# Kernel optimization log

Hardware: AMD Instinct MI355X
Metric: run time of the kernel (lower is better)

The kernel has to match this reference:

```python
import math
import jax, jax.numpy as jnp
import numpy as np

B, T, C, H, V = 2, 512, 768, 12, 50304
HD = C // H
EPS_LN = 1e-5
SINK_ITERS = 6           # MAX_ITER_SINK
N_STEPS = 20             # ceil((1-0)/h_max), h_max=0.05
H_STEP = 1.0 / N_STEPS   # Euler step size h


def layer_norm(x, w, b):
    mu = jnp.mean(x, axis=-1, keepdims=True)
    var = jnp.mean(jnp.square(x - mu), axis=-1, keepdims=True)
    return (x - mu) * jax.lax.rsqrt(var + EPS_LN) * w + b


def sinkhorn_pi(Cmat):
    # log-domain Sinkhorn (eps=1) on cost matrix Cmat [N, T, T]; returns transport plan pi
    n = Cmat.shape[-1]
    log_marg = -jnp.log(jnp.asarray(n, Cmat.dtype))  # log(1/n), uniform marginals
    u = jnp.zeros(Cmat.shape[:-1], Cmat.dtype)
    v = jnp.zeros(Cmat.shape[:-1], Cmat.dtype)
    def M(u, v):
        return -Cmat + u[..., :, None] + v[..., None, :]
    for _ in range(SINK_ITERS):
        u = (log_marg - jax.nn.logsumexp(M(u, v), axis=-1)) + u
        v = (log_marg - jax.nn.logsumexp(M(u, v), axis=-2)) + v
    return jnp.exp(M(u, v))


def block_f(z, t, attn_ln_w, attn_ln_b, c_attn_w, c_attn_b, c_proj_w, c_proj_b,
            mlp_ln_w, mlp_ln_b, c_fc_w, c_fc_b, mlp_proj_w, mlp_proj_b):
    Bz, Tz, Cz = z.shape
    tcol = jnp.full((Bz, Tz, 1), t, z.dtype)
    # attention sub-block: LN over C+1 dims (x concat time)
    x = layer_norm(jnp.concatenate([z, tcol], axis=-1), attn_ln_w, attn_ln_b)
    qkv = x @ c_attn_w + c_attn_b                      # [B,T,3C]
    q, k, v = jnp.split(qkv, 3, axis=-1)
    q = q.reshape(Bz, Tz, H, HD).transpose(0, 2, 1, 3)  # [B,H,T,hd]
    k = k.reshape(Bz, Tz, H, HD).transpose(0, 2, 1, 3)
    v = v.reshape(Bz, Tz, H, HD).transpose(0, 2, 1, 3)
    att = jnp.einsum('bhqd,bhkd->bhqk', q, k) * (1.0 / math.sqrt(HD))
    mask = jnp.tril(jnp.ones((Tz, Tz), dtype=bool))
    att = jax.nn.softmax(jnp.where(mask, att, -jnp.inf), axis=-1)
    pi = sinkhorn_pi(att.reshape(Bz * H, Tz, Tz)) * Tz  # sink(att)[0] * n
    y = jnp.einsum('bhqk,bhkd->bhqd', pi.reshape(Bz, H, Tz, Tz), v)
    y = y.transpose(0, 2, 1, 3).reshape(Bz, Tz, Cz)
    y = y @ c_proj_w + c_proj_b
    # MLP sub-block on LN(concat(attn_out, t))
    ht = layer_norm(jnp.concatenate([y, tcol], axis=-1), mlp_ln_w, mlp_ln_b)
    h1 = jax.nn.gelu(ht @ c_fc_w + c_fc_b, approximate=False)
    return h1 @ mlp_proj_w + mlp_proj_b


def setup_inputs() -> dict:
    key = jax.random.key(0)
    ks = jax.random.split(key, 8)
    s = 0.02
    return {
        'idx': jax.random.randint(ks[0], (B, T), 0, V),
        'wte': s * jax.random.normal(ks[1], (V, C), jnp.float32),
        'wpe': s * jax.random.normal(ks[2], (T, C), jnp.float32),
        'attn_ln_w': jnp.ones((C + 1,), jnp.float32),
        'attn_ln_b': jnp.zeros((C + 1,), jnp.float32),
        'c_attn_w': s * jax.random.normal(ks[3], (C + 1, 3 * C), jnp.float32),
        'c_attn_b': jnp.zeros((3 * C,), jnp.float32),
        'c_proj_w': s * jax.random.normal(ks[4], (C, C), jnp.float32),
        'c_proj_b': jnp.zeros((C,), jnp.float32),
        'mlp_ln_w': jnp.ones((C + 1,), jnp.float32),
        'mlp_ln_b': jnp.zeros((C + 1,), jnp.float32),
        'c_fc_w': s * jax.random.normal(ks[5], (C + 1, 4 * C), jnp.float32),
        'c_fc_b': jnp.zeros((4 * C,), jnp.float32),
        'mlp_proj_w': s * jax.random.normal(ks[6], (4 * C, C), jnp.float32),
        'mlp_proj_b': jnp.zeros((C,), jnp.float32),
        'lnf_w': jnp.ones((C,), jnp.float32),
        'lnf_b': jnp.zeros((C,), jnp.float32),
    }


def reference(idx, wte, wpe, attn_ln_w, attn_ln_b, c_attn_w, c_attn_b, c_proj_w,
              c_proj_b, mlp_ln_w, mlp_ln_b, c_fc_w, c_fc_b, mlp_proj_w, mlp_proj_b,
              lnf_w, lnf_b):
    x = wte[idx] + wpe[jnp.arange(idx.shape[1])]  # [B,T,C]

    def step(carry, _):
        z, t = carry
        dz = block_f(z, t, attn_ln_w, attn_ln_b, c_attn_w, c_attn_b, c_proj_w,
                     c_proj_b, mlp_ln_w, mlp_ln_b, c_fc_w, c_fc_b, mlp_proj_w,
                     mlp_proj_b)
        return (z + H_STEP * dz, t + H_STEP), None

    (x, _), _ = jax.lax.scan(step, (x, jnp.float32(0.0)), None, length=N_STEPS)
    x = layer_norm(x, lnf_w, lnf_b)
    logits = x[:, -1:, :] @ wte.T  # inference path: last position only, tied head
    return logits
```

## Files before the change

### kernel.cpp

```cpp
#include <hip/hip_runtime.h>
#include <hip/hip_bf16.h>
#include <math.h>

typedef unsigned short ushortT;
typedef unsigned int uintT;

#define Bc   2
#define Tc   512
#define Cc   768
#define Hc   12
#define HDc  64
#define Vc   50304
#define BTc  (Bc*Tc)
#define NHc  (Bc*Hc)
#define C3   (3*Cc)
#define C4   (4*Cc)
#define EPS_LN 1e-5f
#define H_STEP 0.05f
#define INVN (1.0f/512.0f)
#define SB   4
#define ELP  (Tc + 8)

typedef float f32x4 __attribute__((ext_vector_type(4)));
typedef __bf16 bf16x8 __attribute__((ext_vector_type(8)));
typedef ushortT us8 __attribute__((ext_vector_type(8)));
typedef uintT u32x4 __attribute__((ext_vector_type(4)));

__device__ __forceinline__ ushortT f2bf(float f) {
    union { float f; unsigned u; } x; x.f = f;
    unsigned r = (x.u + 0x7fffu + ((x.u >> 16) & 1u)) >> 16;
    return (ushortT)r;
}
__device__ __forceinline__ float bf2f(ushortT b) {
    union { unsigned u; float f; } x; x.u = ((unsigned)b) << 16;
    return x.f;
}
__device__ __forceinline__ float bflo(uintT w) {
    union { unsigned u; float f; } x; x.u = w << 16;
    return x.f;
}
__device__ __forceinline__ float bfhi(uintT w) {
    union { unsigned u; float f; } x; x.u = w & 0xffff0000u;
    return x.f;
}

__device__ __forceinline__ void gll16(const ushortT* g, ushortT* l) {
    __builtin_amdgcn_global_load_lds(
        (const __attribute__((address_space(1))) unsigned int*)g,
        (__attribute__((address_space(3))) unsigned int*)l,
        16, 0, 0);
}

__device__ __forceinline__ float waveReduceSumX(float v) {
    for (int o = 32; o; o >>= 1) v += __shfl_xor(v, o);
    return v;
}
__device__ __forceinline__ float blockReduceSum(float v) {
    __shared__ float sm[4];
    for (int o = 32; o; o >>= 1) v += __shfl_down(v, o);
    __syncthreads();
    if ((threadIdx.x & 63) == 0) sm[threadIdx.x >> 6] = v;
    __syncthreads();
    return sm[0] + sm[1] + sm[2] + sm[3];
}

__global__ __launch_bounds__(256)
void wtrans_kernel(const float* __restrict__ W, ushortT* __restrict__ out,
                   int K, int N)
{
    __shared__ float t[32][33];
    int k0 = blockIdx.x * 32, n0 = blockIdx.y * 32;
    int tx = threadIdx.x & 31, ty = threadIdx.x >> 5;
    for (int r = ty; r < 32; r += 8)
        t[r][tx] = W[(size_t)(k0 + r) * N + n0 + tx];
    __syncthreads();
    for (int r = ty; r < 32; r += 8)
        out[(size_t)(n0 + r) * K + k0 + tx] = f2bf(t[tx][r]);
}

__global__ __launch_bounds__(256)
void embed_ln(const int* __restrict__ idx, const float* __restrict__ wte,
              const float* __restrict__ wpe, float* __restrict__ z,
              const float* __restrict__ lnw, const float* __restrict__ lnb,
              ushortT* __restrict__ xlnb, float* __restrict__ xt)
{
    int row = blockIdx.x, tid = threadIdx.x;
    int tok = idx[row];
    float v[3];
#pragma unroll
    for (int q = 0; q < 3; ++q) {
        int c = tid + 256 * q;
        float val = wte[(size_t)tok * Cc + c] + wpe[(size_t)(row & (Tc - 1)) * Cc + c];
        z[(size_t)row * Cc + c] = val;
        v[q] = val;
    }
    float s = blockReduceSum(v[0] + v[1] + v[2]);
    float mu = s / 769.f;
    float d0 = v[0] - mu, d1 = v[1] - mu, d2 = v[2] - mu;
    float ss = blockReduceSum(d0 * d0 + d1 * d1 + d2 * d2);
    float dt = 0.f - mu;
    float var = (ss + dt * dt) / 769.f;
    float rs = rsqrtf(var + EPS_LN);
#pragma unroll
    for (int q = 0; q < 3; ++q) {
        int c = tid + 256 * q;
        xlnb[(size_t)row * Cc + c] = f2bf((v[q] - mu) * rs * lnw[c] + lnb[c]);
    }
    if (tid == 0) xt[row] = dt * rs * lnw[Cc] + lnb[Cc];
}

__global__ __launch_bounds__(256)
void ln_kernel(const void* __restrict__ X, const float* __restrict__ w,
               const float* __restrict__ bb, void* __restrict__ Y,
               float* __restrict__ yt, int hasT, float tval,
               int rowMul, int rowAdd, int obf16, int ibf16)
{
    int orow = blockIdx.x;
    int r = orow * rowMul + rowAdd;
    int tid = threadIdx.x;
    float xv[3];
    if (ibf16) {
        const ushortT* x = (const ushortT*)X + (size_t)r * Cc;
#pragma unroll
        for (int q = 0; q < 3; ++q) xv[q] = bf2f(x[tid + 256 * q]);
    } else {
        const float* x = (const float*)X + (size_t)r * Cc;
#pragma unroll
        for (int q = 0; q < 3; ++q) xv[q] = x[tid + 256 * q];
    }
    float s = blockReduceSum(xv[0] + xv[1] + xv[2]);
    float cnt = hasT ? 769.f : 768.f;
    float mu = (s + (hasT ? tval : 0.f)) / cnt;
    float d0 = xv[0] - mu, d1 = xv[1] - mu, d2 = xv[2] - mu;
    float ss = blockReduceSum(d0 * d0 + d1 * d1 + d2 * d2);
    float dt = tval - mu;
    float var = (ss + (hasT ? dt * dt : 0.f)) / cnt;
    float rs = rsqrtf(var + EPS_LN);
#pragma unroll
    for (int q = 0; q < 3; ++q) {
        int c = tid + 256 * q;
        float v = (xv[q] - mu) * rs * w[c] + bb[c];
        if (obf16) ((ushortT*)Y)[(size_t)orow * Cc + c] = f2bf(v);
        else       ((float*)Y)[(size_t)orow * Cc + c] = v;
    }
    if (hasT && tid == 0) yt[orow] = dt * rs * w[Cc] + bb[Cc];
}

template <int EPI>
__global__ __launch_bounds__(256)
void gemm_bt(const ushortT* __restrict__ A, int lda,
             const ushortT* __restrict__ Bt, int ldb,
             void* __restrict__ Cm, int ldc, int K,
             const float* __restrict__ bias,
             const float* __restrict__ extraA,
             const float* __restrict__ extraB)
{
    __shared__ __align__(16) ushortT Als[128 * 64];
    __shared__ __align__(16) ushortT Bls[128 * 64];
    if (EPI == 4) {
        int koff = blockIdx.z * K;
        A += koff; Bt += koff;
    }
    int tid = threadIdx.x;
    int lane = tid & 63, wid = tid >> 6;
    int wm = wid >> 1, wn = wid & 1;
    int m0 = blockIdx.y * 128, n0 = blockIdx.x * 128;
    f32x4 acc[4][4];
    const f32x4 fz = {0.f, 0.f, 0.f, 0.f};
#pragma unroll
    for (int i = 0; i < 4; ++i)
#pragma unroll
        for (int j = 0; j < 4; ++j) acc[i][j] = fz;

    for (int k0 = 0; k0 < K; k0 += 64) {
#pragma unroll
        for (int is = 0; is < 4; ++is) {
            int ch = is * 256 + tid;
            int m = ch >> 3;
            int kc8 = (ch & 7) ^ (m & 7);
            gll16(A + (size_t)(m0 + m) * lda + k0 + kc8 * 8, Als + ch * 8);
            gll16(Bt + (size_t)(n0 + m) * ldb + k0 + kc8 * 8, Bls + ch * 8);
        }
        __syncthreads();
#pragma unroll
        for (int kk = 0; kk < 2; ++kk) {
            int cidx = kk * 4 + (lane >> 4);
            bf16x8 af[4], bfv[4];
#pragma unroll
            for (int i = 0; i < 4; ++i) {
                int row = wm * 64 + i * 16 + (lane & 15);
                af[i] = *(const bf16x8*)(Als + ((size_t)row * 8 + (cidx ^ (row & 7))) * 8);
                int col = wn * 64 + i * 16 + (lane & 15);
                bfv[i] = *(const bf16x8*)(Bls + ((size_t)col * 8 + (cidx ^ (col & 7))) * 8);
            }
#pragma unroll
            for (int i = 0; i < 4; ++i)
#pragma unroll
                for (int j = 0; j < 4; ++j)
                    acc[i][j] = __builtin_amdgcn_mfma_f32_16x16x32_bf16(af[i], bfv[j], acc[i][j], 0, 0, 0);
        }
        __syncthreads();
    }
#pragma unroll
    for (int i = 0; i < 4; ++i) {
#pragma unroll
        for (int j = 0; j < 4; ++j) {
#pragma unroll
            for (int r = 0; r < 4; ++r) {
                int row = m0 + wm * 64 + i * 16 + (lane >> 4) * 4 + r;
                int col = n0 + wn * 64 + j * 16 + (lane & 15);
                float v = acc[i][j][r];
                if (extraA) v += extraA[row] * extraB[col];
                if (bias) v += bias[col];
                size_t oi = (size_t)row * ldc + col;
                if (EPI == 0) {
                    ((ushortT*)Cm)[oi] = f2bf(v);
                } else if (EPI == 1) {
                    v = 0.5f * v * (1.f + erff(v * 0.70710678118654752440f));
                    ((ushortT*)Cm)[oi] = f2bf(v);
                } else if (EPI == 4) {
                    ((float*)Cm)[(size_t)blockIdx.z * ((size_t)BTc * Cc) + oi] = v;
                }
            }
        }
    }
}

__global__ __launch_bounds__(512)
void sinkfused(const ushortT* __restrict__ qkvb, ushortT* __restrict__ y,
               float* __restrict__ partials, unsigned* __restrict__ ctr,
               unsigned barBase)
{
    int gb = blockIdx.x;
    int n = gb % NHc, r = gb / NHc;
    int row0 = r * 128;
    int b = n / Hc, h = n - b * Hc;
    int tid = threadIdx.x;
    int l = tid & 63, w = tid >> 6;
    __shared__ __align__(16) ushortT Els[128][ELP];
    __shared__ __align__(16) ushortT Kshare[128 * 64];
    __shared__ float a_s[128];
    __shared__ float b_s[Tc];
    const f32x4 fz = {0.f, 0.f, 0.f, 0.f};

    int qrow = b * Tc + row0 + w * 16 + (l & 15);
    const ushortT* qp = qkvb + (size_t)qrow * C3 + h * HDc + (l >> 4) * 8;
    bf16x8 aq0 = *(const bf16x8*)(qp);
    bf16x8 aq1 = *(const bf16x8*)(qp + 32);

    int kcmax = r + 1;
    f32x4 acc[32];
#pragma unroll
    for (int j = 0; j < 32; ++j) acc[j] = fz;

#pragma unroll
    for (int kc = 0; kc < 4; ++kc) {
        if (kc < kcmax) {
            {
                int ch = tid;
                int row = ch >> 3, c16 = (ch & 7) ^ (row & 7);
                gll16(qkvb + (size_t)(b * Tc + kc * 128 + row) * C3 + Cc + h * HDc + c16 * 8,
                      Kshare + ch * 8);
                ch = tid + 512;
                row = ch >> 3; c16 = (ch & 7) ^ (row & 7);
                gll16(qkvb + (size_t)(b * Tc + kc * 128 + row) * C3 + Cc + h * HDc + c16 * 8,
                      Kshare + ch * 8);
            }
            __syncthreads();
#pragma unroll
            for (int jj = 0; jj < 8; ++jj) {
                int krow = jj * 16 + (l & 15);
                int c16a = (l >> 4);
                int c16b = 4 + (l >> 4);
                bf16x8 bk0 = *(const bf16x8*)(Kshare + ((size_t)krow * 8 + (c16a ^ (krow & 7))) * 8);
                bf16x8 bk1 = *(const bf16x8*)(Kshare + ((size_t)krow * 8 + (c16b ^ (krow & 7))) * 8);
                acc[kc * 8 + jj] = __builtin_amdgcn_mfma_f32_16x16x32_bf16(aq0, bk0, acc[kc * 8 + jj], 0, 0, 0);
                acc[kc * 8 + jj] = __builtin_amdgcn_mfma_f32_16x16x32_bf16(aq1, bk1, acc[kc * 8 + jj], 0, 0, 0);
            }
            __syncthreads();
        }
    }

    int nvalid = kcmax * 8;
    int colbase = (l & 15);
    int rowa[4];
#pragma unroll
    for (int e = 0; e < 4; ++e) rowa[e] = row0 + w * 16 + (l >> 4) * 4 + e;

    float mx[4] = {-INFINITY, -INFINITY, -INFINITY, -INFINITY};
#pragma unroll
    for (int j = 0; j < 32; ++j) {
        if (j < nvalid) {
            int col = j * 16 + colbase;
#pragma unroll
            for (int e = 0; e < 4; ++e)
                if (col <= rowa[e]) mx[e] = fmaxf(mx[e], acc[j][e] * 0.125f);
        }
    }
#pragma unroll
    for (int e = 0; e < 4; ++e)
        for (int o = 1; o < 16; o <<= 1) mx[e] = fmaxf(mx[e], __shfl_xor(mx[e], o));

    float se[4] = {0.f, 0.f, 0.f, 0.f};
#pragma unroll
    for (int j = 0; j < 32; ++j) {
        if (j < nvalid) {
            int col = j * 16 + colbase;
#pragma unroll
            for (int e = 0; e < 4; ++e) {
                float exv = (col <= rowa[e]) ? __expf(acc[j][e] * 0.125f - mx[e]) : 0.f;
                acc[j][e] = exv;
                se[e] += exv;
            }
        }
    }
#pragma unroll
    for (int e = 0; e < 4; ++e)
        for (int o = 1; o < 16; o <<= 1) se[e] += __shfl_xor(se[e], o);
    float inv[4];
#pragma unroll
    for (int e = 0; e < 4; ++e) inv[e] = 1.f / se[e];

    float rsum[4] = {0.f, 0.f, 0.f, 0.f};
#pragma unroll
    for (int j = 0; j < 32; ++j) {
        if (j < nvalid) {
            int col = j * 16 + colbase;
#pragma unroll
            for (int e = 0; e < 4; ++e) {
                float Ee = __expf(-(acc[j][e] * inv[e]));
                rsum[e] += Ee;
                Els[w * 16 + (l >> 4) * 4 + e][col] = f2bf(Ee);
            }
        }
    }
#pragma unroll
    for (int e = 0; e < 4; ++e) {
        for (int o = 1; o < 16; o <<= 1) rsum[e] += __shfl_xor(rsum[e], o);
        if ((l & 15) == 0)
            a_s[w * 16 + (l >> 4) * 4 + e] = INVN / (rsum[e] + (float)(Tc - nvalid * 16));
    }
    {
        int tailc = 64 - kcmax * 16;
        if (tailc > 0) {
            us8 ones8;
#pragma unroll
            for (int e = 0; e < 8; ++e) ones8[e] = 0x3F80;
            for (int idx2 = l; idx2 < 16 * tailc; idx2 += 64) {
                int rr = idx2 / tailc, cc = idx2 - rr * tailc;
                *(us8*)&Els[w * 16 + rr][(kcmax * 16 + cc) * 8] = ones8;
            }
        }
    }
    __syncthreads();

    float* mypart = partials + (size_t)(n * SB + r) * Tc;
    const float* hpart = partials + (size_t)n * SB * Tc;
    unsigned* myctr = ctr + n * 16;
    float* scr = (float*)Kshare;

#pragma unroll 1
    for (int p = 0; p < 11; ++p) {
        if ((p & 1) == 0) {
            int cg = tid & 63, sl = tid >> 6;
            float ac[8] = {0.f, 0.f, 0.f, 0.f, 0.f, 0.f, 0.f, 0.f};
#pragma unroll
            for (int i = 0; i < 16; ++i) {
                int row = sl * 16 + i;
                us8 ev = *(const us8*)&Els[row][cg * 8];
                float fa = a_s[row];
#pragma unroll
                for (int e = 0; e < 8; ++e)
                    ac[e] += bf2f(ev[e]) * fa;
            }
            f32x4 lo = {ac[0], ac[1], ac[2], ac[3]};
            f32x4 hi = {ac[4], ac[5], ac[6], ac[7]};
            *(f32x4*)&scr[sl * 512 + cg * 8] = lo;
            *(f32x4*)&scr[sl * 512 + cg * 8 + 4] = hi;
            __syncthreads();
            int j = tid;
            float accs = 0.f;
#pragma unroll
            for (int s2 = 0; s2 < 8; ++s2) accs += scr[s2 * 512 + j];
            __hip_atomic_store(&mypart[j], accs, __ATOMIC_RELAXED, __HIP_MEMORY_SCOPE_AGENT);
            __syncthreads();
            if (tid == 0) {
                __threadfence();
                atomicAdd(myctr, 1u);
                unsigned tgt = barBase + (unsigned)(p / 2 + 1) * SB;
                while (__hip_atomic_load(myctr, __ATOMIC_ACQUIRE, __HIP_MEMORY_SCOPE_AGENT) < tgt)
                    __builtin_amdgcn_s_sleep(2);
            }
            __syncthreads();
            float s0 = __hip_atomic_load(&hpart[j], __ATOMIC_RELAXED, __HIP_MEMORY_SCOPE_AGENT);
            float s1 = __hip_atomic_load(&hpart[Tc + j], __ATOMIC_RELAXED, __HIP_MEMORY_SCOPE_AGENT);
            float s2 = __hip_atomic_load(&hpart[2 * Tc + j], __ATOMIC_RELAXED, __HIP_MEMORY_SCOPE_AGENT);
            float s3 = __hip_atomic_load(&hpart[3 * Tc + j], __ATOMIC_RELAXED, __HIP_MEMORY_SCOPE_AGENT);
            b_s[j] = INVN / (s0 + s1 + s2 + s3);
            __syncthreads();
        } else {
            f32x4 b0 = *(const f32x4*)&b_s[l * 8];
            f32x4 b1 = *(const f32x4*)&b_s[l * 8 + 4];
            float breg[8] = {b0[0], b0[1], b0[2], b0[3], b1[0], b1[1], b1[2], b1[3]};
#pragma unroll 1
            for (int k = 0; k < 16; k += 4) {
                int r0 = w * 16 + k;
                u32x4 q0 = *(const u32x4*)(&Els[r0 + 0][l * 8]);
                u32x4 q1 = *(const u32x4*)(&Els[r0 + 1][l * 8]);
                u32x4 q2 = *(const u32x4*)(&Els[r0 + 2][l * 8]);
                u32x4 q3 = *(const u32x4*)(&Els[r0 + 3][l * 8]);
                float s0 = 0.f, s1 = 0.f, s2 = 0.f, s3 = 0.f;
#pragma unroll
                for (int c = 0; c < 4; ++c) {
                    s0 += bflo(q0[c]) * breg[2 * c] + bfhi(q0[c]) * breg[2 * c + 1];
                    s1 += bflo(q1[c]) * breg[2 * c] + bfhi(q1[c]) * breg[2 * c + 1];
                    s2 += bflo(q2[c]) * breg[2 * c] + bfhi(q2[c]) * breg[2 * c + 1];
                    s3 += bflo(q3[c]) * breg[2 * c] + bfhi(q3[c]) * breg[2 * c + 1];
                }
                s0 = waveReduceSumX(s0);
                s1 = waveReduceSumX(s1);
                s2 = waveReduceSumX(s2);
                s3 = waveReduceSumX(s3);
                if (l == 0) {
                    a_s[r0 + 0] = INVN / s0;
                    a_s[r0 + 1] = INVN / s1;
                    a_s[r0 + 2] = INVN / s2;
                    a_s[r0 + 3] = INVN / s3;
                }
            }
            __syncthreads();
        }
    }

    {
        ushortT* Kls2 = Kshare;
        int wm = w >> 1, wn = w & 1;
        f32x4 acc2[2][2];
#pragma unroll
        for (int i = 0; i < 2; ++i)
#pragma unroll
            for (int j = 0; j < 2; ++j) acc2[i][j] = fz;
        const ushortT* vbase = qkvb + (size_t)(b * Tc) * C3 + 2 * Cc + h * HDc;

#pragma unroll 1
        for (int k0 = 0; k0 < Tc; k0 += 64) {
            {
                int tt = tid >> 3, dblk = tid & 7;
                us8 vv = *(const us8*)(vbase + (size_t)(k0 + tt) * C3 + dblk * 8);
                float bs = 512.f * b_s[k0 + tt];
#pragma unroll
                for (int e = 0; e < 8; ++e)
                    Kls2[(dblk * 8 + e) * 72 + tt] = f2bf(bf2f(vv[e]) * bs);
            }
            __syncthreads();
#pragma unroll
            for (int kk = 0; kk < 64; kk += 32) {
                bf16x8 af[2], bv[2];
#pragma unroll
                for (int i = 0; i < 2; ++i)
                    af[i] = *(const bf16x8*)&Els[wm * 32 + i * 16 + (l & 15)][k0 + kk + (l >> 4) * 8];
#pragma unroll
                for (int j = 0; j < 2; ++j)
                    bv[j] = *(const bf16x8*)(Kls2 + (size_t)(wn * 32 + j * 16 + (l & 15)) * 72 + kk + (l >> 4) * 8);
#pragma unroll
                for (int i = 0; i < 2; ++i)
#pragma unroll
                    for (int j = 0; j < 2; ++j)
                        acc2[i][j] = __builtin_amdgcn_mfma_f32_16x16x32_bf16(af[i], bv[j], acc2[i][j], 0, 0, 0);
            }
            __syncthreads();
        }
#pragma unroll
        for (int i = 0; i < 2; ++i)
#pragma unroll
            for (int j = 0; j < 2; ++j)
#pragma unroll
                for (int rr = 0; rr < 4; ++rr) {
                    int lrow = wm * 32 + i * 16 + (l >> 4) * 4 + rr;
                    float a_r = a_s[lrow];
                    int grow = b * Tc + row0 + lrow;
                    int gcol = h * HDc + wn * 32 + j * 16 + (l & 15);
                    y[(size_t)grow * Cc + gcol] = f2bf(acc2[i][j][rr] * a_r);
                }
    }
}

__global__ __launch_bounds__(256)
void reduce_ln(const float* __restrict__ parts, const float* __restrict__ bias,
               float* __restrict__ z, const float* __restrict__ lnw,
               const float* __restrict__ lnb, ushortT* __restrict__ xlnb,
               float* __restrict__ xt, float tval)
{
    int row = blockIdx.x, tid = threadIdx.x;
    const size_t CS = (size_t)BTc * Cc;
    float v[3];
#pragma unroll
    for (int q = 0; q < 3; ++q) {
        int c = tid + 256 * q;
        size_t idx = (size_t)row * Cc + c;
        float s = parts[idx] + parts[CS + idx] + parts[2 * CS + idx]
                + parts[3 * CS + idx] + bias[c];
        v[q] = z[idx] + H_STEP * s;
        z[idx] = v[q];
    }
    float s = blockReduceSum(v[0] + v[1] + v[2]);
    float mu = (s + tval) / 769.f;
    float d0 = v[0] - mu, d1 = v[1] - mu, d2 = v[2] - mu;
    float ss = blockReduceSum(d0 * d0 + d1 * d1 + d2 * d2);
    float dt = tval - mu;
    float var = (ss + dt * dt) / 769.f;
    float rs = rsqrtf(var + EPS_LN);
#pragma unroll
    for (int q = 0; q < 3; ++q) {
        int c = tid + 256 * q;
        xlnb[(size_t)row * Cc + c] = f2bf((v[q] - mu) * rs * lnw[c] + lnb[c]);
    }
    if (tid == 0) xt[row] = dt * rs * lnw[Cc] + lnb[Cc];
}

__global__ __launch_bounds__(256)
void logits_kernel(const float* __restrict__ xf, const float* __restrict__ wte,
                   float* __restrict__ out)
{
    __shared__ __align__(16) float xs[2 * Cc];
    int tid = threadIdx.x;
    for (int i = tid; i < 384; i += 256)
        ((f32x4*)xs)[i] = ((const f32x4*)xf)[i];
    __syncthreads();
    int w = tid >> 6, lane = tid & 63;
    int vrow = blockIdx.x * 4 + w;
    const f32x4* wr = (const f32x4*)(wte + (size_t)vrow * Cc);
    const f32x4* x0 = (const f32x4*)xs;
    const f32x4* x1 = (const f32x4*)(xs + Cc);
    float a0 = 0.f, a1 = 0.f;
#pragma unroll
    for (int it = 0; it < 3; ++it) {
        int k4 = it * 64 + lane;
        f32x4 wv = wr[k4];
        f32x4 p = x0[k4], q = x1[k4];
        a0 += wv[0] * p[0] + wv[1] * p[1] + wv[2] * p[2] + wv[3] * p[3];
        a1 += wv[0] * q[0] + wv[1] * q[1] + wv[2] * q[2] + wv[3] * q[3];
    }
    for (int o = 32; o; o >>= 1) {
        a0 += __shfl_down(a0, o);
        a1 += __shfl_down(a1, o);
    }
    if (lane == 0) {
        out[vrow] = a0;
        out[Vc + vrow] = a1;
    }
}

extern "C" void kernel_launch(void* const* d_in, const int* in_sizes, int n_in,
                              void* d_out, int out_size, void* d_ws, size_t ws_size,
                              hipStream_t stream)
{
    const int*   idx        = (const int*)  d_in[0];
    const float* wte        = (const float*)d_in[1];
    const float* wpe        = (const float*)d_in[2];
    const float* attn_ln_w  = (const float*)d_in[3];
    const float* attn_ln_b  = (const float*)d_in[4];
    const float* c_attn_w   = (const float*)d_in[5];
    const float* c_attn_b   = (const float*)d_in[6];
    const float* c_proj_w   = (const float*)d_in[7];
    const float* c_proj_b   = (const float*)d_in[8];
    const float* mlp_ln_w   = (const float*)d_in[9];
    const float* mlp_ln_b   = (const float*)d_in[10];
    const float* c_fc_w     = (const float*)d_in[11];
    const float* c_fc_b     = (const float*)d_in[12];
    const float* mlp_proj_w = (const float*)d_in[13];
    const float* mlp_proj_b = (const float*)d_in[14];
    const float* lnf_w      = (const float*)d_in[15];
    const float* lnf_b      = (const float*)d_in[16];
    float* out = (float*)d_out;

    char* base = (char*)d_ws;
    size_t off = 0;
    auto alloc = [&](size_t bytes) -> void* {
        void* p = base + off;
        off = (off + bytes + 255) & ~(size_t)255;
        return p;
    };
    float*   z     = (float*)  alloc((size_t)BTc * Cc * 4);
    float*   parts = (float*)  alloc((size_t)4 * BTc * Cc * 4);
    ushortT* qkvb  = (ushortT*)alloc((size_t)BTc * C3 * 2);
    ushortT* xlnb  = (ushortT*)alloc((size_t)BTc * Cc * 2);
    ushortT* y     = (ushortT*)alloc((size_t)BTc * Cc * 2);
    ushortT* h1    = (ushortT*)alloc((size_t)BTc * C4 * 2);
    ushortT* aob   = (ushortT*)alloc((size_t)BTc * Cc * 2);
    float*   xt    = (float*)  alloc(BTc * 4);
    float*   partv = (float*)  alloc((size_t)NHc * SB * Tc * 4);
    unsigned* ctr  = (unsigned*)alloc(NHc * 16 * 4);
    float*   xf    = (float*)  alloc(2 * Cc * 4);
    ushortT* WqkvT = (ushortT*)alloc((size_t)C3 * Cc * 2);
    ushortT* WprojT= (ushortT*)alloc((size_t)Cc * Cc * 2);
    ushortT* WfcT  = (ushortT*)alloc((size_t)C4 * Cc * 2);
    ushortT* WmlpT = (ushortT*)alloc((size_t)Cc * C4 * 2);

    hipMemsetAsync(ctr, 0, NHc * 16 * 4, stream);
    embed_ln<<<BTc, 256, 0, stream>>>(idx, wte, wpe, z, attn_ln_w, attn_ln_b, xlnb, xt);
    wtrans_kernel<<<dim3(Cc / 32, C3 / 32), 256, 0, stream>>>(c_attn_w,   WqkvT,  Cc, C3);
    wtrans_kernel<<<dim3(Cc / 32, Cc / 32), 256, 0, stream>>>(c_proj_w,   WprojT, Cc, Cc);
    wtrans_kernel<<<dim3(Cc / 32, C4 / 32), 256, 0, stream>>>(c_fc_w,     WfcT,   Cc, C4);
    wtrans_kernel<<<dim3(C4 / 32, Cc / 32), 256, 0, stream>>>(mlp_proj_w, WmlpT,  C4, Cc);

    float t = 0.f;
    for (int step = 0; step < 20; ++step) {
        gemm_bt<0><<<dim3(C3 / 128, BTc / 128), 256, 0, stream>>>(
            xlnb, Cc, WqkvT, Cc, qkvb, C3, Cc,
            c_attn_b, xt, c_attn_w + (size_t)Cc * C3);
        sinkfused<<<NHc * SB, 512, 0, stream>>>(
            qkvb, y, partv, ctr, (unsigned)(step * 6 * SB));
        gemm_bt<0><<<dim3(Cc / 128, BTc / 128), 256, 0, stream>>>(
            y, Cc, WprojT, Cc, aob, Cc, Cc,
            c_proj_b, nullptr, nullptr);
        ln_kernel<<<BTc, 256, 0, stream>>>(aob, mlp_ln_w, mlp_ln_b, xlnb, xt, 1, t, 1, 0, 1, 1);
        gemm_bt<1><<<dim3(C4 / 128, BTc / 128), 256, 0, stream>>>(
            xlnb, Cc, WfcT, Cc, h1, C4, Cc,
            c_fc_b, xt, c_fc_w + (size_t)Cc * C4);
        gemm_bt<4><<<dim3(Cc / 128, BTc / 128, 4), 256, 0, stream>>>(
            h1, C4, WmlpT, C4, parts, Cc, C4 / 4,
            nullptr, nullptr, nullptr);
        t += H_STEP;
        reduce_ln<<<BTc, 256, 0, stream>>>(parts, mlp_proj_b, z,
                                           attn_ln_w, attn_ln_b, xlnb, xt, t);
    }

    ln_kernel<<<2, 256, 0, stream>>>(z, lnf_w, lnf_b, xf, nullptr, 0, 0.f, Tc, Tc - 1, 0, 0);
    logits_kernel<<<Vc / 4, 256, 0, stream>>>(xf, wte, out);
}
```

Baseline: 3.758 ms.

## Split-K the attention projection GEMM and preload all K tiles in sinkfused

The c_proj GEMM now runs split-K in four slices writing fp32 partials, and the existing reduce_ln kernel gains a non-Euler mode that sums the partials, adds the bias and applies the MLP LayerNorm. This replaces the 48-block GEMM plus a separate LN pass, giving four times more blocks on the small GEMM at the cost of extra fp32 partial traffic. Separately, sinkfused loads every needed K chunk into the Els shared buffer up front with one barrier instead of staging one chunk per iteration with two barriers each. That reuses Els before it is needed, which relies on Els being large enough to hold the full K tile set.

```diff
diff --git a/kernel.cpp b/kernel.cpp
--- a/kernel.cpp
+++ b/kernel.cpp
@@ -253,33 +253,32 @@
 #pragma unroll
     for (int j = 0; j < 32; ++j) acc[j] = fz;
 
+    ushortT* EK = &Els[0][0];
+    {
+        int nch = kcmax * 1024;
+        for (int ch = tid; ch < nch; ch += 512) {
+            int row = ch >> 3, c16 = (ch & 7) ^ (row & 7);
+            gll16(qkvb + (size_t)(b * Tc + row) * C3 + Cc + h * HDc + c16 * 8,
+                  EK + ch * 8);
+        }
+    }
+    __syncthreads();
 #pragma unroll
     for (int kc = 0; kc < 4; ++kc) {
         if (kc < kcmax) {
-            {
-                int ch = tid;
-                int row = ch >> 3, c16 = (ch & 7) ^ (row & 7);
-                gll16(qkvb + (size_t)(b * Tc + kc * 128 + row) * C3 + Cc + h * HDc + c16 * 8,
-                      Kshare + ch * 8);
-                ch = tid + 512;
-                row = ch >> 3; c16 = (ch & 7) ^ (row & 7);
-                gll16(qkvb + (size_t)(b * Tc + kc * 128 + row) * C3 + Cc + h * HDc + c16 * 8,
-                      Kshare + ch * 8);
-            }
-            __syncthreads();
 #pragma unroll
             for (int jj = 0; jj < 8; ++jj) {
-                int krow = jj * 16 + (l & 15);
+                int krow = kc * 128 + jj * 16 + (l & 15);
                 int c16a = (l >> 4);
                 int c16b = 4 + (l >> 4);
-                bf16x8 bk0 = *(const bf16x8*)(Kshare + ((size_t)krow * 8 + (c16a ^ (krow & 7))) * 8);
-                bf16x8 bk1 = *(const bf16x8*)(Kshare + ((size_t)krow * 8 + (c16b ^ (krow & 7))) * 8);
+                bf16x8 bk0 = *(const bf16x8*)(EK + ((size_t)krow * 8 + (c16a ^ (krow & 7))) * 8);
+                bf16x8 bk1 = *(const bf16x8*)(EK + ((size_t)krow * 8 + (c16b ^ (krow & 7))) * 8);
                 acc[kc * 8 + jj] = __builtin_amdgcn_mfma_f32_16x16x32_bf16(aq0, bk0, acc[kc * 8 + jj], 0, 0, 0);
                 acc[kc * 8 + jj] = __builtin_amdgcn_mfma_f32_16x16x32_bf16(aq1, bk1, acc[kc * 8 + jj], 0, 0, 0);
             }
-            __syncthreads();
-        }
-    }
+        }
+    }
+    __syncthreads();
 
     int nvalid = kcmax * 8;
     int colbase = (l & 15);
@@ -489,7 +488,7 @@
 void reduce_ln(const float* __restrict__ parts, const float* __restrict__ bias,
                float* __restrict__ z, const float* __restrict__ lnw,
                const float* __restrict__ lnb, ushortT* __restrict__ xlnb,
-               float* __restrict__ xt, float tval)
+               float* __restrict__ xt, float tval, int doEuler)
 {
     int row = blockIdx.x, tid = threadIdx.x;
     const size_t CS = (size_t)BTc * Cc;
@@ -500,8 +499,12 @@
         size_t idx = (size_t)row * Cc + c;
         float s = parts[idx] + parts[CS + idx] + parts[2 * CS + idx]
                 + parts[3 * CS + idx] + bias[c];
-        v[q] = z[idx] + H_STEP * s;
-        z[idx] = v[q];
+        if (doEuler) {
+            v[q] = z[idx] + H_STEP * s;
+            z[idx] = v[q];
+        } else {
+            v[q] = s;
+        }
     }
     float s = blockReduceSum(v[0] + v[1] + v[2]);
     float mu = (s + tval) / 769.f;
@@ -587,7 +590,6 @@
     ushortT* xlnb  = (ushortT*)alloc((size_t)BTc * Cc * 2);
     ushortT* y     = (ushortT*)alloc((size_t)BTc * Cc * 2);
     ushortT* h1    = (ushortT*)alloc((size_t)BTc * C4 * 2);
-    ushortT* aob   = (ushortT*)alloc((size_t)BTc * Cc * 2);
     float*   xt    = (float*)  alloc(BTc * 4);
     float*   partv = (float*)  alloc((size_t)NHc * SB * Tc * 4);
     unsigned* ctr  = (unsigned*)alloc(NHc * 16 * 4);
@@ -611,10 +613,11 @@
             c_attn_b, xt, c_attn_w + (size_t)Cc * C3);
         sinkfused<<<NHc * SB, 512, 0, stream>>>(
             qkvb, y, partv, ctr, (unsigned)(step * 6 * SB));
-        gemm_bt<0><<<dim3(Cc / 128, BTc / 128), 256, 0, stream>>>(
-            y, Cc, WprojT, Cc, aob, Cc, Cc,
-            c_proj_b, nullptr, nullptr);
-        ln_kernel<<<BTc, 256, 0, stream>>>(aob, mlp_ln_w, mlp_ln_b, xlnb, xt, 1, t, 1, 0, 1, 1);
+        gemm_bt<4><<<dim3(Cc / 128, BTc / 128, 4), 256, 0, stream>>>(
+            y, Cc, WprojT, Cc, parts, Cc, Cc / 4,
+            nullptr, nullptr, nullptr);
+        reduce_ln<<<BTc, 256, 0, stream>>>(parts, c_proj_b, nullptr,
+                                           mlp_ln_w, mlp_ln_b, xlnb, xt, t, 0);
         gemm_bt<1><<<dim3(C4 / 128, BTc / 128), 256, 0, stream>>>(
             xlnb, Cc, WfcT, Cc, h1, C4, Cc,
             c_fc_b, xt, c_fc_w + (size_t)Cc * C4);
@@ -623,7 +626,7 @@
             nullptr, nullptr, nullptr);
         t += H_STEP;
         reduce_ln<<<BTc, 256, 0, stream>>>(parts, mlp_proj_b, z,
-                                           attn_ln_w, attn_ln_b, xlnb, xt, t);
+                                           attn_ln_w, attn_ln_b, xlnb, xt, t, 1);
     }
 
     ln_kernel<<<2, 256, 0, stream>>>(z, lnf_w, lnf_b, xf, nullptr, 0, 0.f, Tc, Tc - 1, 0, 0);
```

New measurement: 3.433 ms. 8.7% less time.
